# Optimization experiments

Hardware: AMD Instinct MI355X
Metric: run time of the kernel (lower is better)

Reference implementation:

```python
import jax, jax.numpy as jnp
import numpy as np

D = 4096

def setup_inputs() -> dict:
    key = jax.random.key(0)
    k1, k2 = jax.random.split(key)
    matrix = jax.random.normal(k1, (D, D), dtype=jnp.float32)
    n = jax.random.normal(k2, (D,), dtype=jnp.float32)
    return {"matrix": matrix, "n": n}

def reference(matrix, n):
    # matrix @ matrix.T is PSD; adding a strictly positive softplus diagonal makes it SPD
    m = matrix @ matrix.T + jnp.diag(jax.nn.softplus(n))
    return jnp.linalg.cholesky(m)
```

## Files before the change

### kernel.cpp

```cpp
#include <hip/hip_runtime.h>
#include <math.h>

#define D 4096
#define NB 128
#define KC 32
#define NT (D / NB)
#define LDP 40

typedef __attribute__((ext_vector_type(8))) short short8;
typedef __attribute__((ext_vector_type(4))) float f32x4;
typedef __attribute__((ext_vector_type(4))) unsigned int uint4v;
typedef unsigned short ush;

__device__ __forceinline__ float softplusf(float x) {
  return fmaxf(x, 0.0f) + log1pf(expf(-fabsf(x)));
}

struct HL { unsigned int h, l; };

__device__ __forceinline__ HL split2(float x0, float x1) {
  unsigned int b0 = __float_as_uint(x0), b1 = __float_as_uint(x1);
  unsigned int h0 = b0 & 0xFFFF0000u, h1 = b1 & 0xFFFF0000u;
  float r0 = x0 - __uint_as_float(h0);
  float r1 = x1 - __uint_as_float(h1);
  HL out;
  out.h = h1 | (h0 >> 16);
  out.l = (__float_as_uint(r1) & 0xFFFF0000u) | (__float_as_uint(r0) >> 16);
  return out;
}

__device__ __forceinline__ void split1(float x, ush& h, ush& l) {
  unsigned int b = __float_as_uint(x);
  unsigned int hb = b & 0xFFFF0000u;
  float r = x - __uint_as_float(hb);
  h = (ush)(hb >> 16);
  l = (ush)(__float_as_uint(r) >> 16);
}

__device__ void potrf_factor(float (*Ls)[NB + 1]) {
  int tid = threadIdx.x;
  int lane = tid & 63, wid = tid >> 6;
  int tx = tid & 15, ty = tid >> 4;

  for (int pp = 0; pp < 8; ++pp) {
    int pc0 = pp * 16;
    if (wid == 0) {
      int ra = lane, rb = lane + 64;
      bool va = (ra >= pc0), vb = (rb >= pc0);
      float xa[16], xb[16];
#pragma unroll
      for (int c = 0; c < 16; ++c) {
        xa[c] = va ? Ls[ra][pc0 + c] : 0.0f;
        xb[c] = vb ? Ls[rb][pc0 + c] : 0.0f;
      }
#pragma unroll
      for (int j = 0; j < 16; ++j) {
        int jj = pc0 + j;
        float dv = (jj < 64) ? __shfl(xa[j], jj) : __shfl(xb[j], jj - 64);
        float di = __builtin_amdgcn_rcpf(dv);
        float ta = (ra > jj) ? xa[j] * di : 0.0f;
        float tb = (rb > jj) ? xb[j] * di : 0.0f;
#pragma unroll
        for (int c = j + 1; c < 16; ++c) {
          int rc = pc0 + c;
          float lc = (rc < 64) ? __shfl(xa[j], rc) : __shfl(xb[j], rc - 64);
          xa[c] -= ta * lc;
          xb[c] -= tb * lc;
        }
      }
#pragma unroll
      for (int c = 0; c < 16; ++c) {
        int rc = pc0 + c;
        float dc = (rc < 64) ? __shfl(xa[c], rc) : __shfl(xb[c], rc - 64);
        float sc = __builtin_amdgcn_rsqf(dc);
        xa[c] *= sc;
        xb[c] *= sc;
      }
      if (va) {
#pragma unroll
        for (int c = 0; c < 16; ++c) Ls[ra][pc0 + c] = xa[c];
      }
      if (vb) {
#pragma unroll
        for (int c = 0; c < 16; ++c) Ls[rb][pc0 + c] = xb[c];
      }
    }
    __syncthreads();

    int s0 = pc0 + 16;
    if (s0 < NB) {
      int r0 = ty * 8, c0 = tx * 8;
      if (r0 >= s0 && c0 >= s0) {
        float acc[8][8];
#pragma unroll
        for (int rr = 0; rr < 8; ++rr) {
          float4 m0 = *(const float4*)&Ls[r0 + rr][c0];
          float4 m1 = *(const float4*)&Ls[r0 + rr][c0 + 4];
          acc[rr][0] = m0.x; acc[rr][1] = m0.y; acc[rr][2] = m0.z; acc[rr][3] = m0.w;
          acc[rr][4] = m1.x; acc[rr][5] = m1.y; acc[rr][6] = m1.z; acc[rr][7] = m1.w;
        }
#pragma unroll
        for (int q = 0; q < 16; ++q) {
          float av[8], bv[8];
#pragma unroll
          for (int rr = 0; rr < 8; ++rr) av[rr] = Ls[r0 + rr][pc0 + q];
#pragma unroll
          for (int cc = 0; cc < 8; ++cc) bv[cc] = Ls[c0 + cc][pc0 + q];
#pragma unroll
          for (int rr = 0; rr < 8; ++rr)
#pragma unroll
            for (int cc = 0; cc < 8; ++cc) acc[rr][cc] -= av[rr] * bv[cc];
        }
#pragma unroll
        for (int rr = 0; rr < 8; ++rr) {
          *(float4*)&Ls[r0 + rr][c0] =
              make_float4(acc[rr][0], acc[rr][1], acc[rr][2], acc[rr][3]);
          *(float4*)&Ls[r0 + rr][c0 + 4] =
              make_float4(acc[rr][4], acc[rr][5], acc[rr][6], acc[rr][7]);
        }
      }
    }
    __syncthreads();
  }
}

__device__ void potrf_store(float* Msrc, float (*Ls)[NB + 1]) {
  int tid = threadIdx.x;
  for (int idx = tid; idx < NB * NB; idx += 256) {
    int i = idx >> 7, j = idx & (NB - 1);
    Msrc[(size_t)i * D + j] = (j <= i) ? Ls[i][j] : 0.0f;
  }
}

__global__ __launch_bounds__(256) void potrf_kernel(float* __restrict__ M, int kb)
{
  __shared__ float Ls[NB][NB + 1];
  int tid = threadIdx.x;
  float* Msrc = M + (size_t)kb * D + kb;
  for (int idx = tid; idx < NB * NB; idx += 256) {
    int i = idx >> 7, j = idx & (NB - 1);
    Ls[i][j] = Msrc[(size_t)i * D + j];
  }
  __syncthreads();
  potrf_factor(Ls);
  potrf_store(Msrc, Ls);
}

__global__ __launch_bounds__(256) void convA_kernel(
    const float* __restrict__ A, ush* __restrict__ AhG, ush* __restrict__ AlG)
{
  size_t idx = ((size_t)blockIdx.x * 256 + threadIdx.x) * 8;
  float4 v0 = *(const float4*)(A + idx);
  float4 v1 = *(const float4*)(A + idx + 4);
  HL p0 = split2(v0.x, v0.y), p1 = split2(v0.z, v0.w);
  HL p2 = split2(v1.x, v1.y), p3 = split2(v1.z, v1.w);
  uint4v h = {p0.h, p1.h, p2.h, p3.h};
  uint4v l = {p0.l, p1.l, p2.l, p3.l};
  *(uint4v*)(AhG + idx) = h;
  *(uint4v*)(AlG + idx) = l;
}

template <bool SHA>
__global__ __launch_bounds__(256) void syrk0_kernel(
    const float* __restrict__ Asrc, const float* __restrict__ nvec,
    float* __restrict__ Mout,
    const ush* __restrict__ AhG, const ush* __restrict__ AlG)
{
  __shared__ ush Ah[NB][LDP], Al[NB][LDP];
  __shared__ ush Bh[NB][LDP], Bl[NB][LDP];

  int b = blockIdx.x;
  int ti = (int)((sqrtf(8.0f * (float)b + 1.0f) - 1.0f) * 0.5f);
  while ((ti + 1) * (ti + 2) / 2 <= b) ++ti;
  while (ti * (ti + 1) / 2 > b) --ti;
  int tj = b - ti * (ti + 1) / 2;
  int row0 = ti * NB, col0 = tj * NB;

  int tid = threadIdx.x;
  int lane = tid & 63, wid = tid >> 6;
  int wr = wid >> 1, wc = wid & 1;
  int srow = tid >> 1;
  int scg = (tid & 1) * 16;

  f32x4 acc[4][4];
#pragma unroll
  for (int m = 0; m < 4; ++m)
#pragma unroll
    for (int n = 0; n < 4; ++n) acc[m][n] = (f32x4){0.f, 0.f, 0.f, 0.f};

  int lr16 = lane & 15, kof = (lane >> 4) * 8;

  for (int kk = 0; kk < D; kk += KC) {
    if (SHA) {
      const ush* pah = AhG + (size_t)(row0 + srow) * D + kk + scg;
      const ush* pal = AlG + (size_t)(row0 + srow) * D + kk + scg;
      const ush* pbh = AhG + (size_t)(col0 + srow) * D + kk + scg;
      const ush* pbl = AlG + (size_t)(col0 + srow) * D + kk + scg;
      short8 ah0 = *(const short8*)pah, ah1 = *(const short8*)(pah + 8);
      short8 al0 = *(const short8*)pal, al1 = *(const short8*)(pal + 8);
      short8 bh0 = *(const short8*)pbh, bh1 = *(const short8*)(pbh + 8);
      short8 bl0 = *(const short8*)pbl, bl1 = *(const short8*)(pbl + 8);
      __syncthreads();
      *(short8*)&Ah[srow][scg] = ah0;  *(short8*)&Ah[srow][scg + 8] = ah1;
      *(short8*)&Al[srow][scg] = al0;  *(short8*)&Al[srow][scg + 8] = al1;
      *(short8*)&Bh[srow][scg] = bh0;  *(short8*)&Bh[srow][scg + 8] = bh1;
      *(short8*)&Bl[srow][scg] = bl0;  *(short8*)&Bl[srow][scg + 8] = bl1;
    } else {
      const float* pa = Asrc + (size_t)(row0 + srow) * D + kk + scg;
      const float* pb = Asrc + (size_t)(col0 + srow) * D + kk + scg;
      float4 av0 = *(const float4*)(pa + 0), av1 = *(const float4*)(pa + 4);
      float4 av2 = *(const float4*)(pa + 8), av3 = *(const float4*)(pa + 12);
      float4 bv0 = *(const float4*)(pb + 0), bv1 = *(const float4*)(pb + 4);
      float4 bv2 = *(const float4*)(pb + 8), bv3 = *(const float4*)(pb + 12);
      __syncthreads();
      {
        HL p0 = split2(av0.x, av0.y), p1 = split2(av0.z, av0.w);
        HL p2 = split2(av1.x, av1.y), p3 = split2(av1.z, av1.w);
        HL p4 = split2(av2.x, av2.y), p5 = split2(av2.z, av2.w);
        HL p6 = split2(av3.x, av3.y), p7 = split2(av3.z, av3.w);
        uint4v h0 = {p0.h, p1.h, p2.h, p3.h}, l0 = {p0.l, p1.l, p2.l, p3.l};
        uint4v h1 = {p4.h, p5.h, p6.h, p7.h}, l1 = {p4.l, p5.l, p6.l, p7.l};
        *(uint4v*)&Ah[srow][scg] = h0;  *(uint4v*)&Ah[srow][scg + 8] = h1;
        *(uint4v*)&Al[srow][scg] = l0;  *(uint4v*)&Al[srow][scg + 8] = l1;
      }
      {
        HL p0 = split2(bv0.x, bv0.y), p1 = split2(bv0.z, bv0.w);
        HL p2 = split2(bv1.x, bv1.y), p3 = split2(bv1.z, bv1.w);
        HL p4 = split2(bv2.x, bv2.y), p5 = split2(bv2.z, bv2.w);
        HL p6 = split2(bv3.x, bv3.y), p7 = split2(bv3.z, bv3.w);
        uint4v h0 = {p0.h, p1.h, p2.h, p3.h}, l0 = {p0.l, p1.l, p2.l, p3.l};
        uint4v h1 = {p4.h, p5.h, p6.h, p7.h}, l1 = {p4.l, p5.l, p6.l, p7.l};
        *(uint4v*)&Bh[srow][scg] = h0;  *(uint4v*)&Bh[srow][scg + 8] = h1;
        *(uint4v*)&Bl[srow][scg] = l0;  *(uint4v*)&Bl[srow][scg + 8] = l1;
      }
    }
    __syncthreads();

    short8 ah[4], al[4], bh[4], bl[4];
#pragma unroll
    for (int m = 0; m < 4; ++m) {
      int r = wr * 64 + m * 16 + lr16;
      ah[m] = *(const short8*)&Ah[r][kof];
      al[m] = *(const short8*)&Al[r][kof];
    }
#pragma unroll
    for (int n = 0; n < 4; ++n) {
      int c = wc * 64 + n * 16 + lr16;
      bh[n] = *(const short8*)&Bh[c][kof];
      bl[n] = *(const short8*)&Bl[c][kof];
    }
#pragma unroll
    for (int m = 0; m < 4; ++m)
#pragma unroll
      for (int n = 0; n < 4; ++n) {
        acc[m][n] = __builtin_amdgcn_mfma_f32_16x16x32_bf16(ah[m], bh[n], acc[m][n], 0, 0, 0);
        acc[m][n] = __builtin_amdgcn_mfma_f32_16x16x32_bf16(ah[m], bl[n], acc[m][n], 0, 0, 0);
        acc[m][n] = __builtin_amdgcn_mfma_f32_16x16x32_bf16(al[m], bh[n], acc[m][n], 0, 0, 0);
      }
  }

  int cl = lane & 15, rg = (lane >> 4) * 4;
#pragma unroll
  for (int m = 0; m < 4; ++m) {
#pragma unroll
    for (int n = 0; n < 4; ++n) {
      int gi0 = row0 + wr * 64 + m * 16 + rg;
      int gj = col0 + wc * 64 + n * 16 + cl;
#pragma unroll
      for (int r = 0; r < 4; ++r) {
        int gi = gi0 + r;
        float v = acc[m][n][r];
        if (gi == gj) v += softplusf(nvec[gi]);
        Mout[(size_t)gi * D + gj] = v;
      }
    }
  }

  if (ti > tj) {
    float4 z = make_float4(0.f, 0.f, 0.f, 0.f);
    int zr = tid >> 1;
    int zc0 = (tid & 1) * 64;
    float* zp = Mout + (size_t)(col0 + zr) * D + row0 + zc0;
#pragma unroll
    for (int q = 0; q < 16; ++q) *(float4*)(zp + 4 * q) = z;
  }
}

template <bool SH>
__global__ __launch_bounds__(256) void trsm_kernel(
    float* __restrict__ M, int kb, ush* __restrict__ shH, ush* __restrict__ shL)
{
  __shared__ float Ls[NB][NB + 1];
  __shared__ float dinv[NB];
  int tid = threadIdx.x;
  const float* Lsrc = M + (size_t)kb * D + kb;
  for (int idx = tid; idx < NB * NB; idx += 256) {
    int i = idx >> 7, j = idx & (NB - 1);
    Ls[i][j] = Lsrc[(size_t)i * D + j];
  }
  __syncthreads();
  if (tid < NB) dinv[tid] = 1.0f / Ls[tid][tid];
  __syncthreads();
  int lane = tid & 63, w = tid >> 6;
  size_t r0 = (size_t)(kb + NB) + (size_t)blockIdx.x * 8 + w * 2;
  float* p0 = M + r0 * D + kb;
  float* p1 = p0 + D;
  float x0l = p0[lane], x0h = p0[64 + lane];
  float x1l = p1[lane], x1h = p1[64 + lane];
  for (int p = 0; p < 64; ++p) {
    float dv = dinv[p];
    float xp0 = __shfl(x0l, p) * dv;
    float xp1 = __shfl(x1l, p) * dv;
    float Llo = Ls[lane][p];
    float Lhi = Ls[64 + lane][p];
    if (lane == p)      { x0l = xp0; x1l = xp1; }
    else if (lane > p)  { x0l -= xp0 * Llo; x1l -= xp1 * Llo; }
    x0h -= xp0 * Lhi;
    x1h -= xp1 * Lhi;
  }
  for (int p = 64; p < NB; ++p) {
    int q = p - 64;
    float dv = dinv[p];
    float xp0 = __shfl(x0h, q) * dv;
    float xp1 = __shfl(x1h, q) * dv;
    float Lhi = Ls[64 + lane][p];
    if (lane == q)      { x0h = xp0; x1h = xp1; }
    else if (lane > q)  { x0h -= xp0 * Lhi; x1h -= xp1 * Lhi; }
  }
  p0[lane] = x0l; p0[64 + lane] = x0h;
  p1[lane] = x1l; p1[64 + lane] = x1h;
  if (SH) {
    ush h, l;
    split1(x0l, h, l);
    shH[r0 * NB + lane] = h;        shL[r0 * NB + lane] = l;
    split1(x0h, h, l);
    shH[r0 * NB + 64 + lane] = h;   shL[r0 * NB + 64 + lane] = l;
    split1(x1l, h, l);
    shH[(r0 + 1) * NB + lane] = h;      shL[(r0 + 1) * NB + lane] = l;
    split1(x1h, h, l);
    shH[(r0 + 1) * NB + 64 + lane] = h; shL[(r0 + 1) * NB + 64 + lane] = l;
  }
}

__device__ void gemm_bt(const float* __restrict__ Ap, const float* __restrict__ Bp,
                        f32x4 (&acc)[4][4],
                        ush (*Ah)[LDP], ush (*Al)[LDP],
                        ush (*Bh)[LDP], ush (*Bl)[LDP])
{
  int tid = threadIdx.x;
  int lane = tid & 63, wid = tid >> 6;
  int wr = wid >> 1, wc = wid & 1;
  int srow = tid >> 1, scg = (tid & 1) * 16;
  int lr16 = lane & 15, kof = (lane >> 4) * 8;

  for (int kk = 0; kk < NB; kk += KC) {
    const float* pa = Ap + (size_t)srow * D + kk + scg;
    const float* pb = Bp + (size_t)srow * D + kk + scg;
    float4 av0 = *(const float4*)(pa + 0), av1 = *(const float4*)(pa + 4);
    float4 av2 = *(const float4*)(pa + 8), av3 = *(const float4*)(pa + 12);
    float4 bv0 = *(const float4*)(pb + 0), bv1 = *(const float4*)(pb + 4);
    float4 bv2 = *(const float4*)(pb + 8), bv3 = *(const float4*)(pb + 12);

    __syncthreads();
    {
      HL p0 = split2(av0.x, av0.y), p1 = split2(av0.z, av0.w);
      HL p2 = split2(av1.x, av1.y), p3 = split2(av1.z, av1.w);
      HL p4 = split2(av2.x, av2.y), p5 = split2(av2.z, av2.w);
      HL p6 = split2(av3.x, av3.y), p7 = split2(av3.z, av3.w);
      uint4v h0 = {p0.h, p1.h, p2.h, p3.h}, l0 = {p0.l, p1.l, p2.l, p3.l};
      uint4v h1 = {p4.h, p5.h, p6.h, p7.h}, l1 = {p4.l, p5.l, p6.l, p7.l};
      *(uint4v*)&Ah[srow][scg] = h0;  *(uint4v*)&Ah[srow][scg + 8] = h1;
      *(uint4v*)&Al[srow][scg] = l0;  *(uint4v*)&Al[srow][scg + 8] = l1;
    }
    {
      HL p0 = split2(bv0.x, bv0.y), p1 = split2(bv0.z, bv0.w);
      HL p2 = split2(bv1.x, bv1.y), p3 = split2(bv1.z, bv1.w);
      HL p4 = split2(bv2.x, bv2.y), p5 = split2(bv2.z, bv2.w);
      HL p6 = split2(bv3.x, bv3.y), p7 = split2(bv3.z, bv3.w);
      uint4v h0 = {p0.h, p1.h, p2.h, p3.h}, l0 = {p0.l, p1.l, p2.l, p3.l};
      uint4v h1 = {p4.h, p5.h, p6.h, p7.h}, l1 = {p4.l, p5.l, p6.l, p7.l};
      *(uint4v*)&Bh[srow][scg] = h0;  *(uint4v*)&Bh[srow][scg + 8] = h1;
      *(uint4v*)&Bl[srow][scg] = l0;  *(uint4v*)&Bl[srow][scg + 8] = l1;
    }
    __syncthreads();

    short8 ah[4], al[4], bh[4], bl[4];
#pragma unroll
    for (int m = 0; m < 4; ++m) {
      int r = wr * 64 + m * 16 + lr16;
      ah[m] = *(const short8*)&Ah[r][kof];
      al[m] = *(const short8*)&Al[r][kof];
    }
#pragma unroll
    for (int n = 0; n < 4; ++n) {
      int c = wc * 64 + n * 16 + lr16;
      bh[n] = *(const short8*)&Bh[c][kof];
      bl[n] = *(const short8*)&Bl[c][kof];
    }
#pragma unroll
    for (int m = 0; m < 4; ++m)
#pragma unroll
      for (int n = 0; n < 4; ++n) {
        acc[m][n] = __builtin_amdgcn_mfma_f32_16x16x32_bf16(ah[m], bh[n], acc[m][n], 0, 0, 0);
        acc[m][n] = __builtin_amdgcn_mfma_f32_16x16x32_bf16(ah[m], bl[n], acc[m][n], 0, 0, 0);
        acc[m][n] = __builtin_amdgcn_mfma_f32_16x16x32_bf16(al[m], bh[n], acc[m][n], 0, 0, 0);
      }
  }
}

__device__ void gemm_bt_sh(const ush* __restrict__ AhG, const ush* __restrict__ AlG,
                           const ush* __restrict__ BhG, const ush* __restrict__ BlG,
                           f32x4 (&acc)[4][4],
                           ush (*Ah)[LDP], ush (*Al)[LDP],
                           ush (*Bh)[LDP], ush (*Bl)[LDP])
{
  int tid = threadIdx.x;
  int lane = tid & 63, wid = tid >> 6;
  int wr = wid >> 1, wc = wid & 1;
  int srow = tid >> 1, scg = (tid & 1) * 16;
  int lr16 = lane & 15, kof = (lane >> 4) * 8;

  for (int kk = 0; kk < NB; kk += KC) {
    const ush* pah = AhG + (size_t)srow * NB + kk + scg;
    const ush* pal = AlG + (size_t)srow * NB + kk + scg;
    const ush* pbh = BhG + (size_t)srow * NB + kk + scg;
    const ush* pbl = BlG + (size_t)srow * NB + kk + scg;
    short8 vah0 = *(const short8*)(pah), vah1 = *(const short8*)(pah + 8);
    short8 val0 = *(const short8*)(pal), val1 = *(const short8*)(pal + 8);
    short8 vbh0 = *(const short8*)(pbh), vbh1 = *(const short8*)(pbh + 8);
    short8 vbl0 = *(const short8*)(pbl), vbl1 = *(const short8*)(pbl + 8);

    __syncthreads();
    *(short8*)&Ah[srow][scg] = vah0;  *(short8*)&Ah[srow][scg + 8] = vah1;
    *(short8*)&Al[srow][scg] = val0;  *(short8*)&Al[srow][scg + 8] = val1;
    *(short8*)&Bh[srow][scg] = vbh0;  *(short8*)&Bh[srow][scg + 8] = vbh1;
    *(short8*)&Bl[srow][scg] = vbl0;  *(short8*)&Bl[srow][scg + 8] = vbl1;
    __syncthreads();

    short8 ah[4], al[4], bh[4], bl[4];
#pragma unroll
    for (int m = 0; m < 4; ++m) {
      int r = wr * 64 + m * 16 + lr16;
      ah[m] = *(const short8*)&Ah[r][kof];
      al[m] = *(const short8*)&Al[r][kof];
    }
#pragma unroll
    for (int n = 0; n < 4; ++n) {
      int c = wc * 64 + n * 16 + lr16;
      bh[n] = *(const short8*)&Bh[c][kof];
      bl[n] = *(const short8*)&Bl[c][kof];
    }
#pragma unroll
    for (int m = 0; m < 4; ++m)
#pragma unroll
      for (int n = 0; n < 4; ++n) {
        acc[m][n] = __builtin_amdgcn_mfma_f32_16x16x32_bf16(ah[m], bh[n], acc[m][n], 0, 0, 0);
        acc[m][n] = __builtin_amdgcn_mfma_f32_16x16x32_bf16(ah[m], bl[n], acc[m][n], 0, 0, 0);
        acc[m][n] = __builtin_amdgcn_mfma_f32_16x16x32_bf16(al[m], bh[n], acc[m][n], 0, 0, 0);
      }
  }
}

__global__ __launch_bounds__(256) void syrk_col_kernel(
    float* __restrict__ M, int k0,
    const ush* __restrict__ shH, const ush* __restrict__ shL)
{
  __shared__ __align__(16) unsigned char smem[66560];
  ush (*Ah)[LDP] = (ush(*)[LDP])(smem);
  ush (*Al)[LDP] = (ush(*)[LDP])(smem + 10240);
  ush (*Bh)[LDP] = (ush(*)[LDP])(smem + 20480);
  ush (*Bl)[LDP] = (ush(*)[LDP])(smem + 30720);
  float (*Ls)[NB + 1] = (float(*)[NB + 1])smem;

  int jcol = k0 + 1;
  int i = jcol + blockIdx.x;

  int tid = threadIdx.x;
  int lane = tid & 63, wid = tid >> 6;
  int wr = wid >> 1, wc = wid & 1;
  int cl = lane & 15, rg = (lane >> 4) * 4;

  f32x4 acc[4][4];
#pragma unroll
  for (int m = 0; m < 4; ++m)
#pragma unroll
    for (int n = 0; n < 4; ++n) acc[m][n] = (f32x4){0.f, 0.f, 0.f, 0.f};

  size_t ra = (size_t)(i * NB) * NB;
  size_t rb = (size_t)(jcol * NB) * NB;
  gemm_bt_sh(shH + ra, shL + ra, shH + rb, shL + rb, acc, Ah, Al, Bh, Bl);

  float* Mt = M + (size_t)(i * NB) * D + jcol * NB;
  if (blockIdx.x == 0) {
    __syncthreads();
#pragma unroll
    for (int m = 0; m < 4; ++m)
#pragma unroll
      for (int n = 0; n < 4; ++n) {
        int li0 = wr * 64 + m * 16 + rg;
        int lj = wc * 64 + n * 16 + cl;
#pragma unroll
        for (int r = 0; r < 4; ++r)
          Ls[li0 + r][lj] = Mt[(size_t)(li0 + r) * D + lj] - acc[m][n][r];
      }
    __syncthreads();
    potrf_factor(Ls);
    potrf_store(Mt, Ls);
    return;
  }
#pragma unroll
  for (int m = 0; m < 4; ++m)
#pragma unroll
    for (int n = 0; n < 4; ++n) {
      int li0 = wr * 64 + m * 16 + rg;
      int lj = wc * 64 + n * 16 + cl;
#pragma unroll
      for (int r = 0; r < 4; ++r)
        Mt[(size_t)(li0 + r) * D + lj] -= acc[m][n][r];
    }
}

__global__ __launch_bounds__(256) void syrk256_kernel(
    float* __restrict__ M, int k0,
    const ush* __restrict__ shHE, const ush* __restrict__ shLE,
    const ush* __restrict__ shHO, const ush* __restrict__ shLO)
{
  __shared__ __align__(16) unsigned char smem[66560];
  ush (*Ah)[LDP] = (ush(*)[LDP])(smem);
  ush (*Al)[LDP] = (ush(*)[LDP])(smem + 10240);
  ush (*Bh)[LDP] = (ush(*)[LDP])(smem + 20480);
  ush (*Bl)[LDP] = (ush(*)[LDP])(smem + 30720);
  float (*Ls)[NB + 1] = (float(*)[NB + 1])smem;

  int base = k0 + 2;
  int s = blockIdx.x;
  int tp = (int)((sqrtf(8.0f * (float)s + 1.0f) - 1.0f) * 0.5f);
  while ((tp + 1) * (tp + 2) / 2 <= s) ++tp;
  while (tp * (tp + 1) / 2 > s) --tp;
  int tq = s - tp * (tp + 1) / 2;
  int i = base + tp, j = base + tq;

  int tid = threadIdx.x;
  int lane = tid & 63, wid = tid >> 6;
  int wr = wid >> 1, wc = wid & 1;
  int cl = lane & 15, rg = (lane >> 4) * 4;

  f32x4 acc[4][4];
#pragma unroll
  for (int m = 0; m < 4; ++m)
#pragma unroll
    for (int n = 0; n < 4; ++n) acc[m][n] = (f32x4){0.f, 0.f, 0.f, 0.f};

  size_t ra = (size_t)(i * NB) * NB;
  size_t rb = (size_t)(j * NB) * NB;
  gemm_bt_sh(shHE + ra, shLE + ra, shHE + rb, shLE + rb, acc, Ah, Al, Bh, Bl);
  gemm_bt_sh(shHO + ra, shLO + ra, shHO + rb, shLO + rb, acc, Ah, Al, Bh, Bl);

  float* Mt = M + (size_t)(i * NB) * D + j * NB;
  if (s == 0) {
    __syncthreads();
#pragma unroll
    for (int m = 0; m < 4; ++m)
#pragma unroll
      for (int n = 0; n < 4; ++n) {
        int li0 = wr * 64 + m * 16 + rg;
        int lj = wc * 64 + n * 16 + cl;
#pragma unroll
        for (int r = 0; r < 4; ++r)
          Ls[li0 + r][lj] = Mt[(size_t)(li0 + r) * D + lj] - acc[m][n][r];
      }
    __syncthreads();
    potrf_factor(Ls);
    potrf_store(Mt, Ls);
    return;
  }
#pragma unroll
  for (int m = 0; m < 4; ++m)
#pragma unroll
    for (int n = 0; n < 4; ++n) {
      int li0 = wr * 64 + m * 16 + rg;
      int lj = wc * 64 + n * 16 + cl;
#pragma unroll
      for (int r = 0; r < 4; ++r)
        Mt[(size_t)(li0 + r) * D + lj] -= acc[m][n][r];
    }
}

__global__ __launch_bounds__(256) void syrk1_fb_kernel(float* __restrict__ M, int kb)
{
  __shared__ __align__(16) unsigned char smem[66560];
  ush (*Ah)[LDP] = (ush(*)[LDP])(smem);
  ush (*Al)[LDP] = (ush(*)[LDP])(smem + 10240);
  ush (*Bh)[LDP] = (ush(*)[LDP])(smem + 20480);
  ush (*Bl)[LDP] = (ush(*)[LDP])(smem + 30720);
  float (*Ls)[NB + 1] = (float(*)[NB + 1])smem;

  float* Mout = M + (size_t)(kb + NB) * D + (kb + NB);
  const float* Xsrc = M + (size_t)(kb + NB) * D + kb;

  int s = blockIdx.x;
  int ti = (int)((sqrtf(8.0f * (float)s + 1.0f) - 1.0f) * 0.5f);
  while ((ti + 1) * (ti + 2) / 2 <= s) ++ti;
  while (ti * (ti + 1) / 2 > s) --ti;
  int tj = s - ti * (ti + 1) / 2;
  int row0 = ti * NB, col0 = tj * NB;

  int tid = threadIdx.x;
  int lane = tid & 63, wid = tid >> 6;
  int wr = wid >> 1, wc = wid & 1;
  int cl = lane & 15, rg = (lane >> 4) * 4;

  f32x4 acc[4][4];
#pragma unroll
  for (int m = 0; m < 4; ++m)
#pragma unroll
    for (int n = 0; n < 4; ++n) acc[m][n] = (f32x4){0.f, 0.f, 0.f, 0.f};

  gemm_bt(Xsrc + (size_t)row0 * D, Xsrc + (size_t)col0 * D, acc, Ah, Al, Bh, Bl);

  if (s == 0) {
    __syncthreads();
#pragma unroll
    for (int m = 0; m < 4; ++m)
#pragma unroll
      for (int n = 0; n < 4; ++n) {
        int li0 = wr * 64 + m * 16 + rg;
        int lj = wc * 64 + n * 16 + cl;
#pragma unroll
        for (int r = 0; r < 4; ++r)
          Ls[li0 + r][lj] = Mout[(size_t)(li0 + r) * D + lj] - acc[m][n][r];
      }
    __syncthreads();
    potrf_factor(Ls);
    potrf_store(Mout, Ls);
    return;
  }
#pragma unroll
  for (int m = 0; m < 4; ++m)
#pragma unroll
    for (int n = 0; n < 4; ++n) {
      int gi0 = row0 + wr * 64 + m * 16 + rg;
      int gj = col0 + wc * 64 + n * 16 + cl;
#pragma unroll
      for (int r = 0; r < 4; ++r)
        Mout[(size_t)(gi0 + r) * D + gj] -= acc[m][n][r];
    }
}

extern "C" void kernel_launch(void* const* d_in, const int* in_sizes, int n_in,
                              void* d_out, int out_size, void* d_ws, size_t ws_size,
                              hipStream_t stream)
{
  (void)in_sizes; (void)n_in; (void)out_size;
  const float* A  = (const float*)d_in[0];
  const float* nv = (const float*)d_in[1];
  float* M = (float*)d_out;

  const size_t bank = (size_t)D * NB;
  const size_t ash_elems = (size_t)D * D;
  const size_t need_x = 4 * bank * sizeof(ush);
  const size_t need_a = need_x + 2 * ash_elems * sizeof(ush);
  bool shX = (ws_size >= need_x);
  bool shA = (ws_size >= need_a);
  ush* xHE = (ush*)d_ws;
  ush* xLE = xHE + bank;
  ush* xHO = xLE + bank;
  ush* xLO = xHO + bank;
  ush* aH  = xLO + bank;
  ush* aL  = aH + ash_elems;

  if (shA) {
    convA_kernel<<<(int)(ash_elems / 8 / 256), 256, 0, stream>>>(A, aH, aL);
    syrk0_kernel<true><<<NT * (NT + 1) / 2, 256, 0, stream>>>(A, nv, M, aH, aL);
  } else {
    syrk0_kernel<false><<<NT * (NT + 1) / 2, 256, 0, stream>>>(A, nv, M, nullptr, nullptr);
  }
  potrf_kernel<<<1, 256, 0, stream>>>(M, 0);

  if (shX) {
    for (int p = 0; p < NT / 2; ++p) {
      int k0 = 2 * p, kb0 = k0 * NB;
      int T0 = D - kb0 - NB;
      trsm_kernel<true><<<T0 / 8, 256, 0, stream>>>(M, kb0, xHE, xLE);
      int t1 = NT - 1 - k0;
      syrk_col_kernel<<<t1, 256, 0, stream>>>(M, k0, xHE, xLE);
      int T1 = D - (k0 + 1) * NB - NB;
      if (T1 > 0)
        trsm_kernel<true><<<T1 / 8, 256, 0, stream>>>(M, (k0 + 1) * NB, xHO, xLO);
      int t2 = NT - 2 - k0;
      if (t2 > 0) {
        int C2 = t2 * (t2 + 1) / 2;
        syrk256_kernel<<<C2, 256, 0, stream>>>(M, k0, xHE, xLE, xHO, xLO);
      }
    }
  } else {
    for (int k = 0; k <= 30; ++k) {
      int kb = k * NB;
      int T = D - kb - NB;
      int t = T / NB;
      trsm_kernel<false><<<T / 8, 256, 0, stream>>>(M, kb, nullptr, nullptr);
      syrk1_fb_kernel<<<t * (t + 1) / 2, 256, 0, stream>>>(M, kb);
    }
  }
}
```

Baseline: 3.755 ms.

## Batch four panels per trailing SYRK with in-group panel updates

Restructures the blocked Cholesky schedule so the trailing symmetric update runs once per group of four 128-column panels instead of once per two. Inside a group, a new panel-update kernel applies each freshly solved panel only to the remaining columns of the same group and factors the next diagonal block. The big SYRK then accumulates four split-bf16 panel banks in one pass, giving a deeper K per tile. This is meant to cut the number of full trailing-matrix read-modify-write passes and launches, at the cost of more sequential small launches within each group. The panel banks now reuse the workspace that held the converted A, which is only needed by the first SYRK.

```diff
diff --git a/kernel.cpp b/kernel.cpp
--- a/kernel.cpp
+++ b/kernel.cpp
@@ -461,8 +461,8 @@
   }
 }
 
-__global__ __launch_bounds__(256) void syrk_col_kernel(
-    float* __restrict__ M, int k0,
+__global__ __launch_bounds__(256) void panel_update_kernel(
+    float* __restrict__ M, int k, int pend,
     const ush* __restrict__ shH, const ush* __restrict__ shL)
 {
   __shared__ __align__(16) unsigned char smem[66560];
@@ -472,8 +472,11 @@
   ush (*Bl)[LDP] = (ush(*)[LDP])(smem + 30720);
   float (*Ls)[NB + 1] = (float(*)[NB + 1])smem;
 
-  int jcol = k0 + 1;
-  int i = jcol + blockIdx.x;
+  int s = blockIdx.x;
+  int j = k + 1, rem = s;
+  while (rem >= NT - j) { rem -= NT - j; ++j; }
+  int i = j + rem;
+  (void)pend;
 
   int tid = threadIdx.x;
   int lane = tid & 63, wid = tid >> 6;
@@ -487,11 +490,11 @@
     for (int n = 0; n < 4; ++n) acc[m][n] = (f32x4){0.f, 0.f, 0.f, 0.f};
 
   size_t ra = (size_t)(i * NB) * NB;
-  size_t rb = (size_t)(jcol * NB) * NB;
+  size_t rb = (size_t)(j * NB) * NB;
   gemm_bt_sh(shH + ra, shL + ra, shH + rb, shL + rb, acc, Ah, Al, Bh, Bl);
 
-  float* Mt = M + (size_t)(i * NB) * D + jcol * NB;
-  if (blockIdx.x == 0) {
+  float* Mt = M + (size_t)(i * NB) * D + j * NB;
+  if (s == 0) {
     __syncthreads();
 #pragma unroll
     for (int m = 0; m < 4; ++m)
@@ -520,10 +523,12 @@
     }
 }
 
-__global__ __launch_bounds__(256) void syrk256_kernel(
-    float* __restrict__ M, int k0,
-    const ush* __restrict__ shHE, const ush* __restrict__ shLE,
-    const ush* __restrict__ shHO, const ush* __restrict__ shLO)
+__global__ __launch_bounds__(256) void syrk4_kernel(
+    float* __restrict__ M, int base,
+    const ush* __restrict__ h0, const ush* __restrict__ l0,
+    const ush* __restrict__ h1, const ush* __restrict__ l1,
+    const ush* __restrict__ h2, const ush* __restrict__ l2,
+    const ush* __restrict__ h3, const ush* __restrict__ l3)
 {
   __shared__ __align__(16) unsigned char smem[66560];
   ush (*Ah)[LDP] = (ush(*)[LDP])(smem);
@@ -532,7 +537,6 @@
   ush (*Bl)[LDP] = (ush(*)[LDP])(smem + 30720);
   float (*Ls)[NB + 1] = (float(*)[NB + 1])smem;
 
-  int base = k0 + 2;
   int s = blockIdx.x;
   int tp = (int)((sqrtf(8.0f * (float)s + 1.0f) - 1.0f) * 0.5f);
   while ((tp + 1) * (tp + 2) / 2 <= s) ++tp;
@@ -553,8 +557,10 @@
 
   size_t ra = (size_t)(i * NB) * NB;
   size_t rb = (size_t)(j * NB) * NB;
-  gemm_bt_sh(shHE + ra, shLE + ra, shHE + rb, shLE + rb, acc, Ah, Al, Bh, Bl);
-  gemm_bt_sh(shHO + ra, shLO + ra, shHO + rb, shLO + rb, acc, Ah, Al, Bh, Bl);
+  gemm_bt_sh(h0 + ra, l0 + ra, h0 + rb, l0 + rb, acc, Ah, Al, Bh, Bl);
+  gemm_bt_sh(h1 + ra, l1 + ra, h1 + rb, l1 + rb, acc, Ah, Al, Bh, Bl);
+  gemm_bt_sh(h2 + ra, l2 + ra, h2 + rb, l2 + rb, acc, Ah, Al, Bh, Bl);
+  gemm_bt_sh(h3 + ra, l3 + ra, h3 + rb, l3 + rb, acc, Ah, Al, Bh, Bl);
 
   float* Mt = M + (size_t)(i * NB) * D + j * NB;
   if (s == 0) {
@@ -656,44 +662,43 @@
   const float* nv = (const float*)d_in[1];
   float* M = (float*)d_out;
 
+  const size_t ash_elems = (size_t)D * D;
   const size_t bank = (size_t)D * NB;
-  const size_t ash_elems = (size_t)D * D;
-  const size_t need_x = 4 * bank * sizeof(ush);
-  const size_t need_a = need_x + 2 * ash_elems * sizeof(ush);
-  bool shX = (ws_size >= need_x);
-  bool shA = (ws_size >= need_a);
-  ush* xHE = (ush*)d_ws;
-  ush* xLE = xHE + bank;
-  ush* xHO = xLE + bank;
-  ush* xLO = xHO + bank;
-  ush* aH  = xLO + bank;
-  ush* aL  = aH + ash_elems;
+  const size_t need = 2 * ash_elems * sizeof(ush);
+  bool shA = (ws_size >= need);
+  ush* aH = (ush*)d_ws;
+  ush* aL = aH + ash_elems;
+  ush* bk[8];
+  for (int q = 0; q < 8; ++q) bk[q] = (ush*)d_ws + q * bank;
 
   if (shA) {
     convA_kernel<<<(int)(ash_elems / 8 / 256), 256, 0, stream>>>(A, aH, aL);
     syrk0_kernel<true><<<NT * (NT + 1) / 2, 256, 0, stream>>>(A, nv, M, aH, aL);
+    potrf_kernel<<<1, 256, 0, stream>>>(M, 0);
+
+    for (int p = 0; p < 8; ++p) {
+      int pend = 4 * p + 3;
+      for (int q = 0; q < 4; ++q) {
+        int k = 4 * p + q;
+        if (k > 30) break;
+        int T = D - k * NB - NB;
+        trsm_kernel<true><<<T / 8, 256, 0, stream>>>(M, k * NB, bk[2 * q], bk[2 * q + 1]);
+        if (q < 3) {
+          int npu = 0;
+          for (int j = k + 1; j <= pend; ++j) npu += NT - j;
+          panel_update_kernel<<<npu, 256, 0, stream>>>(M, k, pend, bk[2 * q], bk[2 * q + 1]);
+        }
+      }
+      if (p < 7) {
+        int base = 4 * (p + 1);
+        int t2 = NT - base;
+        syrk4_kernel<<<t2 * (t2 + 1) / 2, 256, 0, stream>>>(
+            M, base, bk[0], bk[1], bk[2], bk[3], bk[4], bk[5], bk[6], bk[7]);
+      }
+    }
   } else {
     syrk0_kernel<false><<<NT * (NT + 1) / 2, 256, 0, stream>>>(A, nv, M, nullptr, nullptr);
-  }
-  potrf_kernel<<<1, 256, 0, stream>>>(M, 0);
-
-  if (shX) {
-    for (int p = 0; p < NT / 2; ++p) {
-      int k0 = 2 * p, kb0 = k0 * NB;
-      int T0 = D - kb0 - NB;
-      trsm_kernel<true><<<T0 / 8, 256, 0, stream>>>(M, kb0, xHE, xLE);
-      int t1 = NT - 1 - k0;
-      syrk_col_kernel<<<t1, 256, 0, stream>>>(M, k0, xHE, xLE);
-      int T1 = D - (k0 + 1) * NB - NB;
-      if (T1 > 0)
-        trsm_kernel<true><<<T1 / 8, 256, 0, stream>>>(M, (k0 + 1) * NB, xHO, xLO);
-      int t2 = NT - 2 - k0;
-      if (t2 > 0) {
-        int C2 = t2 * (t2 + 1) / 2;
-        syrk256_kernel<<<C2, 256, 0, stream>>>(M, k0, xHE, xLE, xHO, xLO);
-      }
-    }
-  } else {
+    potrf_kernel<<<1, 256, 0, stream>>>(M, 0);
     for (int k = 0; k <= 30; ++k) {
       int kb = k * NB;
       int T = D - kb - NB;
```

New measurement: 3.753 ms. About the same (-0.1%).
